# Performance work log

Hardware: AMD Instinct MI355X
Metric: run time of the kernel (lower is better)

The kernel has to match this reference:

```python
import jax, jax.numpy as jnp
import numpy as np

C = 256      # dim_in == dim_out (residual add requires it)
H = 96
W = 96
Z = 16       # number of (isWithin, dist) pairs
MAXL = 8


def setup_inputs() -> dict:
    key = jax.random.key(0)
    ks = jax.random.split(key, 8)
    x = jax.random.normal(ks[0], (1, C, H, W), jnp.float32)
    # 1x1 convs without bias == channel matmuls with weight [out_ch, in_ch]
    Wq = jax.random.normal(ks[1], (C, C), jnp.float32) / np.sqrt(C).astype(np.float32)
    Wk = jax.random.normal(ks[2], (C, C), jnp.float32) / np.sqrt(C).astype(np.float32)
    Wv = jax.random.normal(ks[3], (C, C), jnp.float32) / np.sqrt(C).astype(np.float32)
    embd = jax.random.normal(ks[4], (2, 2 * MAXL + 1, C), jnp.float32)  # N(0,1) as in torch
    Wproj = jax.random.normal(ks[5], (C, C + 1), jnp.float32) / np.sqrt(C + 1).astype(np.float32)
    dist = jax.random.randint(ks[6], (Z,), 0, 2 * MAXL + 1) - MAXL      # in [-maxl, maxl]
    isWithin = jax.random.randint(ks[7], (Z,), 0, 2)                     # in {0, 1}
    return {"x": x, "Wq": Wq, "Wk": Wk, "Wv": Wv, "embd": embd,
            "Wproj": Wproj, "dist": dist, "isWithin": isWithin}


def reference(x, Wq, Wk, Wv, embd, Wproj, dist, isWithin):
    b, c, hh, ww = x.shape
    n = hh * ww
    maxl = (embd.shape[1] - 1) // 2
    xf = x.reshape(b, c, n)                                  # [b, c, n]
    q = jnp.einsum('oc,bcn->bon', Wq, xf)                    # 1x1 conv == channel matmul
    k = jnp.einsum('oc,bcn->bon', Wk, xf)
    v = jnp.einsum('oc,bcn->bon', Wv, xf)
    # full (unscaled) attention over spatial tokens, softmax along q axis
    att = jax.nn.softmax(jnp.einsum('bck,bcq->bkq', k, q), axis=-1)  # [b, n, n]
    Y = jnp.einsum('bkq,bck->bcq', att, v)                   # [b, c, n]
    out = Y.reshape(b, c, hh, ww) + x                        # residual
    # relative-distance embedding gather: [z, c]
    rel = embd[isWithin, dist + maxl]
    pos = jnp.einsum('zc,bcn->bzn', rel, xf)                 # [b, z, n] (u=1 folded)
    pos = pos.reshape(b * pos.shape[1], 1, hh, ww)           # [(b z), 1, hh, ww]
    z = pos.shape[0]
    out_rep = jnp.tile(out, (z, 1, 1, 1))                    # [z, c, hh, ww] (b == 1)
    cat = jnp.concatenate([out_rep, pos], axis=1)            # [z, c+1, hh, ww]
    return jnp.einsum('oc,zchw->zohw', Wproj, cat)           # final 1x1 conv
```

## Files before the change

### kernel.cpp

```cpp
#include <hip/hip_runtime.h>
#include <hip/hip_bf16.h>

typedef __bf16 bf8 __attribute__((ext_vector_type(8)));
typedef __bf16 bfx4 __attribute__((ext_vector_type(4)));
typedef float f4 __attribute__((ext_vector_type(4)));

#define NTOK 9216
#define CDIM 256
#define LOG2E 1.44269504f
#define PSHIFT 32.0f

__device__ inline bf8 ldfrag(const __bf16* p, int ld) {
  int l = threadIdx.x & 63;
  return *reinterpret_cast<const bf8*>(p + (l & 15) * ld + ((l >> 4) << 3));
}
__device__ inline f4 mfma16(bf8 a, bf8 b, f4 c) {
  return __builtin_amdgcn_mfma_f32_16x16x32_bf16(a, b, c, 0, 0, 0);
}
__device__ inline void gl2lds(const __bf16* g, __bf16* l) {
  __builtin_amdgcn_global_load_lds(
      (const __attribute__((address_space(1))) void*)g,
      (__attribute__((address_space(3))) void*)l, 16, 0, 0);
}

template <int EPI>
__global__ __launch_bounds__(256) void gemm128(const __bf16* __restrict__ A, int lda,
                                               const __bf16* __restrict__ Bt, int ldb,
                                               void* __restrict__ Cv, int ldc, int K,
                                               const float* __restrict__ aux0,
                                               const float* __restrict__ aux1) {
  __shared__ __bf16 As[128 * 32];
  __shared__ __bf16 Bs[128 * 32];
  const int tid = threadIdx.x;
  const int w = tid >> 6, lane = tid & 63;
  const int lc = lane & 15, quad = lane >> 4;
  const int m0 = blockIdx.x * 128, n0 = blockIdx.y * 128;
  const int wm = (w & 1) << 6, wn = (w >> 1) << 6;
  const int r0 = (w * 2) * 16 + (lane >> 2);
  const int cg = (lane & 3) * 8;
  const __bf16* gA0 = A + (size_t)(m0 + r0) * lda + cg;
  const __bf16* gA1 = A + (size_t)(m0 + r0 + 16) * lda + cg;
  const __bf16* gB0 = Bt + (size_t)(n0 + r0) * ldb + cg;
  const __bf16* gB1 = Bt + (size_t)(n0 + r0 + 16) * ldb + cg;
  __bf16* lA0 = As + (w * 2) * 512;
  __bf16* lA1 = As + (w * 2 + 1) * 512;
  __bf16* lB0 = Bs + (w * 2) * 512;
  __bf16* lB1 = Bs + (w * 2 + 1) * 512;

  f4 acc[4][4] = {};
  for (int kk = 0; kk < K; kk += 32) {
    __syncthreads();
    gl2lds(gA0 + kk, lA0);
    gl2lds(gA1 + kk, lA1);
    gl2lds(gB0 + kk, lB0);
    gl2lds(gB1 + kk, lB1);
    __syncthreads();
    bf8 af[4], bfr[4];
    for (int i = 0; i < 4; i++) af[i] = ldfrag(As + (wm + 16 * i) * 32, 32);
    for (int j = 0; j < 4; j++) bfr[j] = ldfrag(Bs + (wn + 16 * j) * 32, 32);
    for (int i = 0; i < 4; i++)
      for (int j = 0; j < 4; j++) acc[i][j] = mfma16(af[i], bfr[j], acc[i][j]);
  }
  if (EPI == 3) {
    __bf16* Pp = (__bf16*)Cv;
    float* Pd = (float*)aux0;
    const int mb = blockIdx.x * 2 + (w & 1);
    for (int j = 0; j < 4; j++) {
      int col = n0 + wn + 16 * j + lc;
      int sb = col >> 5, c2 = (col >> 3) & 3, e3 = col & 7;
      float d = 0.f;
      for (int i = 0; i < 4; i++) {
        int qb = m0 + wm + 16 * i + quad * 4;
        for (int r = 0; r < 4; r++) {
          float e = exp2f(acc[i][j][r] - PSHIFT);
          d += e;
          Pp[((size_t)sb * NTOK + qb + r) * 32 + ((c2 ^ r) << 3) + e3] = (__bf16)e;
        }
      }
      d += __shfl_xor(d, 16);
      d += __shfl_xor(d, 32);
      if (quad == 0) Pd[(size_t)col * 144 + mb] = d;
    }
  } else if (EPI == 4) {
    float* outp = (float*)Cv;
    for (int i = 0; i < 4; i++)
      for (int r = 0; r < 4; r++) {
        int o = m0 + wm + 16 * i + quad * 4 + r;
        float wo = aux1[o];
        for (int j = 0; j < 4; j++) {
          int n = n0 + wn + 16 * j + lc;
          float b = acc[i][j][r];
          for (int z = 0; z < 16; z++)
            outp[((size_t)z * 256 + o) * NTOK + n] =
                b + wo * aux0[(size_t)z * NTOK + n];
        }
      }
  } else {
    for (int i = 0; i < 4; i++)
      for (int j = 0; j < 4; j++)
        for (int r = 0; r < 4; r++) {
          size_t idx = (size_t)(m0 + wm + 16 * i + quad * 4 + r) * ldc +
                       (n0 + wn + 16 * j + lc);
          ((__bf16*)Cv)[idx] = (__bf16)acc[i][j][r];
        }
  }
}

__global__ __launch_bounds__(256) void prep_kernel(
    const float* Wq, const float* Wk, const float* Wv, const float* embd,
    const float* Wproj, const int* dist, const int* isWithin,
    __bf16* Wqkb, __bf16* Wvb, __bf16* Wpb, float* wl, __bf16* rel) {
  int tid = blockIdx.x * 256 + threadIdx.x;
  if (tid < 65536) {
    Wqkb[tid] = (__bf16)(Wq[tid] * LOG2E);
    Wqkb[65536 + tid] = (__bf16)Wk[tid];
    Wvb[tid] = (__bf16)Wv[tid];
    int o = tid >> 8, c = tid & 255;
    Wpb[tid] = (__bf16)Wproj[o * 257 + c];
    if (c == 0) wl[o] = Wproj[o * 257 + 256];
  }
  if (tid < 16 * 256) {
    int z = tid >> 8, c = tid & 255;
    rel[tid] = (__bf16)embd[(isWithin[z] * 17 + dist[z] + 8) * 256 + c];
  }
}

__global__ __launch_bounds__(256) void transpose_kernel(const float* x, __bf16* Xt) {
  __shared__ __bf16 tile[32][33];
  int n0 = blockIdx.x * 32;
  int c0 = blockIdx.y * 32;
  int tx = threadIdx.x & 31, ty = threadIdx.x >> 5;
  for (int i = 0; i < 32; i += 8)
    tile[ty + i][tx] = (__bf16)x[(c0 + ty + i) * NTOK + n0 + tx];
  __syncthreads();
  for (int i = 0; i < 32; i += 8)
    Xt[(n0 + ty + i) * CDIM + c0 + tx] = tile[tx][ty + i];
}

__global__ __launch_bounds__(256) void gemm_pos(const __bf16* rel, const __bf16* Xt,
                                                float* pos) {
  int n0 = blockIdx.x * 256 + (threadIdx.x >> 6) * 64;
  f4 acc[4] = {};
  for (int ks = 0; ks < 256; ks += 32) {
    bf8 a = ldfrag(rel + ks, 256);
    for (int j = 0; j < 4; j++) {
      bf8 b = ldfrag(Xt + (n0 + 16 * j) * 256 + ks, 256);
      acc[j] = mfma16(a, b, acc[j]);
    }
  }
  int l = threadIdx.x & 63, lc = l & 15, quad = l >> 4;
  for (int j = 0; j < 4; j++)
    for (int r = 0; r < 4; r++)
      pos[(quad * 4 + r) * NTOK + n0 + 16 * j + lc] = acc[j][r];
}

__global__ __launch_bounds__(256) void combine_stats(const float* __restrict__ Pd,
                                                     float* dinv) {
  int kt = blockIdx.x * 4 + (threadIdx.x >> 6);
  int lane = threadIdx.x & 63;
  const float* pd = Pd + (size_t)kt * 144;
  float d = pd[lane] + pd[lane + 64] + ((lane < 16) ? pd[lane + 128] : 0.f);
  for (int off = 1; off < 64; off <<= 1) d += __shfl_xor(d, off);
  if (lane == 0) dinv[kt] = 1.0f / d;
}

__global__ __launch_bounds__(256) void vscale_kernel(const __bf16* __restrict__ V,
                                                     const float* __restrict__ dinv,
                                                     __bf16* __restrict__ Vs) {
  size_t off = ((size_t)blockIdx.x * 256 + threadIdx.x) * 8;
  bf8 v = *reinterpret_cast<const bf8*>(V + off);
  int c = (int)(off / NTOK);
  int kt = (int)(off % NTOK);
  f4 dl = *reinterpret_cast<const f4*>(dinv + kt);
  f4 dh = *reinterpret_cast<const f4*>(dinv + kt + 4);
  bf8 o;
  for (int j = 0; j < 4; j++) o[j] = (__bf16)((float)v[j] * dl[j]);
  for (int j = 0; j < 4; j++) o[4 + j] = (__bf16)((float)v[4 + j] * dh[j]);
  int c2 = (kt >> 3) & 3;
  size_t dst = (size_t)c * NTOK + (kt & ~31) + (((c2 ^ (c & 3))) << 3);
  *reinterpret_cast<bf8*>(Vs + dst) = o;
}

template <int NSTEP>
__global__ __launch_bounds__(256) void pv_kernel(const __bf16* __restrict__ P,
                                                 const __bf16* __restrict__ Vp,
                                                 float* __restrict__ Ypart) {
  __shared__ __bf16 As[3][64 * 32];
  __shared__ __bf16 Bs[3][256 * 32];
  const int tid = threadIdx.x;
  const int w = tid >> 6, lane = tid & 63;
  const int lc = lane & 15, quad = lane >> 4;
  const int q0 = blockIdx.x * 64;
  const int z = blockIdx.y;
  const int wn = w << 6;
  const int sb0 = z * NSTEP;
  const __bf16* gA = P + ((size_t)sb0 * NTOK + q0) * 32 + w * 512 + lane * 8;
  const size_t aStride = (size_t)NTOK * 32;
  const __bf16* gB = Vp + (size_t)(w * 64 + (lane >> 2)) * NTOK + sb0 * 32 +
                     ((lane & 3) << 3);

  for (int p = 0; p < 2; p++) {
    gl2lds(gA + (size_t)p * aStride, &As[p][w * 512]);
    for (int u = 0; u < 4; u++)
      gl2lds(gB + (size_t)(16 * u) * NTOK + p * 32, &Bs[p][(w * 64 + 16 * u) * 32]);
  }

  f4 acc[4][4] = {};
  int cur = 0;
  const int swz = (quad ^ (lc & 3)) << 3;
  for (int s = 0; s < NSTEP; s++) {
    asm volatile("s_waitcnt vmcnt(5)" ::: "memory");
    __builtin_amdgcn_sched_barrier(0);
    __builtin_amdgcn_s_barrier();
    __builtin_amdgcn_sched_barrier(0);
    int sp = (s + 2 < NSTEP) ? s + 2 : NSTEP - 1;
    int nb = cur + 2;
    if (nb >= 3) nb -= 3;
    gl2lds(gA + (size_t)sp * aStride, &As[nb][w * 512]);
    for (int u = 0; u < 4; u++)
      gl2lds(gB + (size_t)(16 * u) * NTOK + sp * 32, &Bs[nb][(w * 64 + 16 * u) * 32]);
    __builtin_amdgcn_sched_barrier(0);
    bf8 af[4], bfr[4];
    for (int i = 0; i < 4; i++)
      af[i] = *reinterpret_cast<const bf8*>(&As[cur][(16 * i + lc) * 32 + swz]);
    for (int j = 0; j < 4; j++)
      bfr[j] = *reinterpret_cast<const bf8*>(&Bs[cur][(wn + 16 * j + lc) * 32 + swz]);
    for (int i = 0; i < 4; i++)
      for (int j = 0; j < 4; j++) acc[i][j] = mfma16(af[i], bfr[j], acc[i][j]);
    cur = cur + 1;
    if (cur >= 3) cur = 0;
  }

  float* Yp = Ypart + (size_t)z * NTOK * 256;
  for (int i = 0; i < 4; i++)
    for (int j = 0; j < 4; j++)
      for (int r = 0; r < 4; r++)
        Yp[(size_t)(q0 + 16 * i + quad * 4 + r) * 256 + wn + 16 * j + lc] =
            acc[i][j][r];
}

__global__ __launch_bounds__(256) void combine_y_kernel(const float* __restrict__ Ypart,
                                                        const __bf16* __restrict__ Xt,
                                                        __bf16* outT, int zp) {
  int i = blockIdx.x * 256 + threadIdx.x;
  f4 y = {};
  for (int z = 0; z < zp; z++) {
    f4 p = reinterpret_cast<const f4*>(Ypart + (size_t)z * NTOK * 256)[i];
    for (int t = 0; t < 4; t++) y[t] += p[t];
  }
  bfx4 xv = reinterpret_cast<const bfx4*>(Xt)[i];
  bfx4 o;
  for (int t = 0; t < 4; t++) o[t] = (__bf16)(y[t] + (float)xv[t]);
  reinterpret_cast<bfx4*>(outT)[i] = o;
}

extern "C" void kernel_launch(void* const* d_in, const int* in_sizes, int n_in,
                              void* d_out, int out_size, void* d_ws, size_t ws_size,
                              hipStream_t stream) {
  const float* x = (const float*)d_in[0];
  const float* Wq = (const float*)d_in[1];
  const float* Wk = (const float*)d_in[2];
  const float* Wv = (const float*)d_in[3];
  const float* embd = (const float*)d_in[4];
  const float* Wproj = (const float*)d_in[5];
  const int* dist = (const int*)d_in[6];
  const int* isW = (const int*)d_in[7];
  float* out = (float*)d_out;

  char* w8 = (char*)d_ws;
  __bf16* Xt = (__bf16*)(w8 + 0);
  __bf16* QKt = (__bf16*)(w8 + 4718592);
  __bf16* V = (__bf16*)(w8 + 14155776);
  __bf16* Wqkb = (__bf16*)(w8 + 18874368);
  __bf16* Wvb = (__bf16*)(w8 + 19136512);
  __bf16* Wpb = (__bf16*)(w8 + 19267584);
  __bf16* rel = (__bf16*)(w8 + 19398656);
  float* wl = (float*)(w8 + 19406848);
  float* pos = (float*)(w8 + 19407872);
  float* dinv = (float*)(w8 + 20034560);
  __bf16* Vs = (__bf16*)(w8 + 20971520);
  const size_t sOff = 29508608;
  __bf16* P = (__bf16*)(w8 + sOff);
  float* Pd = (float*)(w8 + sOff + 171966464);
  const size_t ypOff = sOff + 171966464 + 5308416;
  float* Ypart = (float*)(w8 + ypOff);
  __bf16* outT = (__bf16*)(w8 + sOff);

  static const int ZPS[] = {6, 4, 3, 2, 1};
  int zp = 1;
  for (int i = 0; i < 5; i++)
    if (ypOff + (size_t)ZPS[i] * 9437184 <= ws_size) { zp = ZPS[i]; break; }

  prep_kernel<<<256, 256, 0, stream>>>(Wq, Wk, Wv, embd, Wproj, dist, isW,
                                       Wqkb, Wvb, Wpb, wl, rel);
  transpose_kernel<<<dim3(288, 8), 256, 0, stream>>>(x, Xt);
  gemm128<1><<<dim3(72, 4), 256, 0, stream>>>(Xt, 256, Wqkb, 256, QKt, 512, 256,
                                              nullptr, nullptr);
  gemm128<1><<<dim3(2, 72), 256, 0, stream>>>(Wvb, 256, Xt, 256, V, NTOK, 256,
                                              nullptr, nullptr);
  gemm_pos<<<36, 256, 0, stream>>>(rel, Xt, pos);
  gemm128<3><<<dim3(72, 72), 256, 0, stream>>>(QKt, 512, QKt + 256, 512, P, 0, 256,
                                               (const float*)Pd, nullptr);
  combine_stats<<<2304, 256, 0, stream>>>(Pd, dinv);
  vscale_kernel<<<1152, 256, 0, stream>>>(V, dinv, Vs);
  switch (zp) {
    case 6: pv_kernel<48><<<dim3(144, 6), 256, 0, stream>>>(P, Vs, Ypart); break;
    case 4: pv_kernel<72><<<dim3(144, 4), 256, 0, stream>>>(P, Vs, Ypart); break;
    case 3: pv_kernel<96><<<dim3(144, 3), 256, 0, stream>>>(P, Vs, Ypart); break;
    case 2: pv_kernel<144><<<dim3(144, 2), 256, 0, stream>>>(P, Vs, Ypart); break;
    default: pv_kernel<288><<<dim3(144, 1), 256, 0, stream>>>(P, Vs, Ypart); break;
  }
  combine_y_kernel<<<2304, 256, 0, stream>>>(Ypart, Xt, outT, zp);
  gemm128<4><<<dim3(2, 72), 256, 0, stream>>>(Wpb, 256, outT, 256, out, NTOK, 256,
                                              pos, wl);
}
```

Before: 408.2 us.

## Stage softmax P tile through LDS for coalesced stores; split final projection across z

The QK^T epilogue now writes exp values into shared memory with an XOR swizzle, in two halves, then each thread stores 16-byte vectors of the P tile to global memory. This replaces scattered 2-byte stores. The final projection GEMM also gets a third grid dimension of 4, so each block writes only 4 of the 16 z outputs, which gives more parallelism for the large output write. The cost is extra barriers and LDS reuse in the epilogue, and the projection GEMM is recomputed 4 times.

```diff
diff --git a/kernel.cpp b/kernel.cpp
--- a/kernel.cpp
+++ b/kernel.cpp
@@ -29,8 +29,9 @@
                                                void* __restrict__ Cv, int ldc, int K,
                                                const float* __restrict__ aux0,
                                                const float* __restrict__ aux1) {
-  __shared__ __bf16 As[128 * 32];
-  __shared__ __bf16 Bs[128 * 32];
+  __shared__ __attribute__((aligned(16))) __bf16 smem[8192];
+  __bf16* As = smem;
+  __bf16* Bs = smem + 4096;
   const int tid = threadIdx.x;
   const int w = tid >> 6, lane = tid & 63;
   const int lc = lane & 15, quad = lane >> 4;
@@ -65,24 +66,39 @@
     __bf16* Pp = (__bf16*)Cv;
     float* Pd = (float*)aux0;
     const int mb = blockIdx.x * 2 + (w & 1);
-    for (int j = 0; j < 4; j++) {
-      int col = n0 + wn + 16 * j + lc;
-      int sb = col >> 5, c2 = (col >> 3) & 3, e3 = col & 7;
-      float d = 0.f;
-      for (int i = 0; i < 4; i++) {
-        int qb = m0 + wm + 16 * i + quad * 4;
-        for (int r = 0; r < 4; r++) {
-          float e = exp2f(acc[i][j][r] - PSHIFT);
-          d += e;
-          Pp[((size_t)sb * NTOK + qb + r) * 32 + ((c2 ^ r) << 3) + e3] = (__bf16)e;
+    for (int p = 0; p < 2; p++) {
+      __syncthreads();
+      if ((w & 1) == p) {
+        for (int j = 0; j < 4; j++) {
+          int cl = wn + 16 * j + lc;
+          int sb = cl >> 5, c2 = (cl >> 3) & 3, e3 = cl & 7;
+          float d = 0.f;
+          for (int i = 0; i < 4; i++)
+            for (int r = 0; r < 4; r++) {
+              float e = exp2f(acc[i][j][r] - PSHIFT);
+              d += e;
+              int rl = 16 * i + quad * 4 + r;
+              smem[rl * 128 + ((sb ^ (r & 3)) << 5) + ((c2 ^ (r & 3)) << 3) + e3] =
+                  (__bf16)e;
+            }
+          d += __shfl_xor(d, 16);
+          d += __shfl_xor(d, 32);
+          if (quad == 0) Pd[(size_t)(n0 + cl) * 144 + mb] = d;
         }
       }
-      d += __shfl_xor(d, 16);
-      d += __shfl_xor(d, 32);
-      if (quad == 0) Pd[(size_t)col * 144 + mb] = d;
+      __syncthreads();
+      int rl = tid >> 2, e = tid & 3;
+      for (int sb = 0; sb < 4; sb++) {
+        bf8 v = *reinterpret_cast<const bf8*>(
+            &smem[rl * 128 + ((sb ^ (rl & 3)) << 5) + e * 8]);
+        *reinterpret_cast<bf8*>(
+            Pp + ((size_t)((n0 >> 5) + sb) * NTOK + m0 + p * 64 + rl) * 32 + e * 8) =
+            v;
+      }
     }
   } else if (EPI == 4) {
     float* outp = (float*)Cv;
+    const int z0 = blockIdx.z * 4;
     for (int i = 0; i < 4; i++)
       for (int r = 0; r < 4; r++) {
         int o = m0 + wm + 16 * i + quad * 4 + r;
@@ -90,7 +106,7 @@
         for (int j = 0; j < 4; j++) {
           int n = n0 + wn + 16 * j + lc;
           float b = acc[i][j][r];
-          for (int z = 0; z < 16; z++)
+          for (int z = z0; z < z0 + 4; z++)
             outp[((size_t)z * 256 + o) * NTOK + n] =
                 b + wo * aux0[(size_t)z * NTOK + n];
         }
@@ -311,6 +327,6 @@
     default: pv_kernel<288><<<dim3(144, 1), 256, 0, stream>>>(P, Vs, Ypart); break;
   }
   combine_y_kernel<<<2304, 256, 0, stream>>>(Ypart, Xt, outT, zp);
-  gemm128<4><<<dim3(2, 72), 256, 0, stream>>>(Wpb, 256, outT, 256, out, NTOK, 256,
-                                              pos, wl);
-}
+  gemm128<4><<<dim3(2, 72, 4), 256, 0, stream>>>(Wpb, 256, outT, 256, out, NTOK, 256,
+                                                 pos, wl);
+}
```

Measured after the change: 416.7 us. 2.1% more time.

## Add pipelined score GEMM with transposed operands and split output GEMM over z

Applied to the files above, without the earlier changes.

Replaces the generic score GEMM epilogue with a dedicated kernel that triple-buffers LDS loads through async global-to-LDS copies and keeps up to two stages in flight. Operands are swapped so each lane writes four exponentials as one packed vector store, and denominators are reduced across lanes in registers. The final projection GEMM grid gains a z dimension of four, so each block writes four z slices and the launch has more parallelism. The cost is extra LDS use and a recomputed projection GEMM in each z block.

```diff
diff --git a/kernel.cpp b/kernel.cpp
--- a/kernel.cpp
+++ b/kernel.cpp
@@ -61,28 +61,9 @@
     for (int i = 0; i < 4; i++)
       for (int j = 0; j < 4; j++) acc[i][j] = mfma16(af[i], bfr[j], acc[i][j]);
   }
-  if (EPI == 3) {
-    __bf16* Pp = (__bf16*)Cv;
-    float* Pd = (float*)aux0;
-    const int mb = blockIdx.x * 2 + (w & 1);
-    for (int j = 0; j < 4; j++) {
-      int col = n0 + wn + 16 * j + lc;
-      int sb = col >> 5, c2 = (col >> 3) & 3, e3 = col & 7;
-      float d = 0.f;
-      for (int i = 0; i < 4; i++) {
-        int qb = m0 + wm + 16 * i + quad * 4;
-        for (int r = 0; r < 4; r++) {
-          float e = exp2f(acc[i][j][r] - PSHIFT);
-          d += e;
-          Pp[((size_t)sb * NTOK + qb + r) * 32 + ((c2 ^ r) << 3) + e3] = (__bf16)e;
-        }
-      }
-      d += __shfl_xor(d, 16);
-      d += __shfl_xor(d, 32);
-      if (quad == 0) Pd[(size_t)col * 144 + mb] = d;
-    }
-  } else if (EPI == 4) {
+  if (EPI == 4) {
     float* outp = (float*)Cv;
+    const int z0 = blockIdx.z * 4;
     for (int i = 0; i < 4; i++)
       for (int r = 0; r < 4; r++) {
         int o = m0 + wm + 16 * i + quad * 4 + r;
@@ -90,7 +71,7 @@
         for (int j = 0; j < 4; j++) {
           int n = n0 + wn + 16 * j + lc;
           float b = acc[i][j][r];
-          for (int z = 0; z < 16; z++)
+          for (int z = z0; z < z0 + 4; z++)
             outp[((size_t)z * 256 + o) * NTOK + n] =
                 b + wo * aux0[(size_t)z * NTOK + n];
         }
@@ -103,6 +84,95 @@
                        (n0 + wn + 16 * j + lc);
           ((__bf16*)Cv)[idx] = (__bf16)acc[i][j][r];
         }
+  }
+}
+
+__global__ __launch_bounds__(256) void sgemm_kernel(const __bf16* __restrict__ Kt,
+                                                    const __bf16* __restrict__ Qt,
+                                                    __bf16* __restrict__ Pp,
+                                                    float* __restrict__ Pd) {
+  __shared__ __bf16 As[3][128 * 32];
+  __shared__ __bf16 Bs[3][128 * 32];
+  const int tid = threadIdx.x;
+  const int w = tid >> 6, lane = tid & 63;
+  const int lc = lane & 15, quad = lane >> 4;
+  const int m0 = blockIdx.x * 128;
+  const int n0 = blockIdx.y * 128;
+  const int wm = (w & 1) << 6, wn = (w >> 1) << 6;
+  const int r0 = w * 32 + (lane >> 2);
+  const int cg = (lane & 3) * 8;
+  const __bf16* gA0 = Kt + (size_t)(m0 + r0) * 512 + cg;
+  const __bf16* gA1 = Kt + (size_t)(m0 + r0 + 16) * 512 + cg;
+  const __bf16* gB0 = Qt + (size_t)(n0 + r0) * 512 + cg;
+  const __bf16* gB1 = Qt + (size_t)(n0 + r0 + 16) * 512 + cg;
+  const int la = w * 1024;
+
+  for (int p = 0; p < 2; p++) {
+    gl2lds(gA0 + p * 32, &As[p][la]);
+    gl2lds(gA1 + p * 32, &As[p][la + 512]);
+    gl2lds(gB0 + p * 32, &Bs[p][la]);
+    gl2lds(gB1 + p * 32, &Bs[p][la + 512]);
+  }
+
+  f4 acc[4][4] = {};
+  int cur = 0;
+  for (int s = 0; s < 8; s++) {
+    asm volatile("s_waitcnt vmcnt(4)" ::: "memory");
+    __builtin_amdgcn_sched_barrier(0);
+    __builtin_amdgcn_s_barrier();
+    __builtin_amdgcn_sched_barrier(0);
+    int sp = (s + 2 < 8) ? s + 2 : 7;
+    int nb = cur + 2;
+    if (nb >= 3) nb -= 3;
+    gl2lds(gA0 + sp * 32, &As[nb][la]);
+    gl2lds(gA1 + sp * 32, &As[nb][la + 512]);
+    gl2lds(gB0 + sp * 32, &Bs[nb][la]);
+    gl2lds(gB1 + sp * 32, &Bs[nb][la + 512]);
+    __builtin_amdgcn_sched_barrier(0);
+    bf8 af[4], bfr[4];
+    for (int i = 0; i < 4; i++) af[i] = ldfrag(&As[cur][(wm + 16 * i) * 32], 32);
+    for (int j = 0; j < 4; j++) bfr[j] = ldfrag(&Bs[cur][(wn + 16 * j) * 32], 32);
+    for (int i = 0; i < 4; i++)
+      for (int j = 0; j < 4; j++) acc[i][j] = mfma16(af[i], bfr[j], acc[i][j]);
+    cur = cur + 1;
+    if (cur >= 3) cur = 0;
+  }
+
+  float dsum[4][4];
+  for (int i = 0; i < 4; i++)
+    for (int r = 0; r < 4; r++) dsum[i][r] = 0.f;
+  for (int j = 0; j < 4; j++) {
+    int q = n0 + wn + 16 * j + lc;
+    for (int i = 0; i < 4; i++) {
+      int ktb = m0 + wm + 16 * i;
+      int c2 = ((i & 1) << 1) | (quad >> 1);
+      bfx4 pk;
+      for (int r = 0; r < 4; r++) {
+        float e = exp2f(acc[i][j][r] - PSHIFT);
+        dsum[i][r] += e;
+        pk[r] = (__bf16)e;
+      }
+      __bf16* dst = Pp + ((size_t)(ktb >> 5) * NTOK + q) * 32 +
+                    ((c2 ^ (lc & 3)) << 3) + ((quad & 1) << 2);
+      *reinterpret_cast<bfx4*>(dst) = pk;
+    }
+  }
+  for (int i = 0; i < 4; i++)
+    for (int r = 0; r < 4; r++) {
+      float d = dsum[i][r];
+      d += __shfl_xor(d, 1);
+      d += __shfl_xor(d, 2);
+      d += __shfl_xor(d, 4);
+      d += __shfl_xor(d, 8);
+      dsum[i][r] = d;
+    }
+  if (lc == 0) {
+    int mb = blockIdx.y * 2 + (w >> 1);
+    for (int i = 0; i < 4; i++)
+      for (int r = 0; r < 4; r++) {
+        int kt = m0 + wm + 16 * i + quad * 4 + r;
+        Pd[(size_t)kt * 144 + mb] = dsum[i][r];
+      }
   }
 }
 
@@ -299,8 +369,7 @@
   gemm128<1><<<dim3(2, 72), 256, 0, stream>>>(Wvb, 256, Xt, 256, V, NTOK, 256,
                                               nullptr, nullptr);
   gemm_pos<<<36, 256, 0, stream>>>(rel, Xt, pos);
-  gemm128<3><<<dim3(72, 72), 256, 0, stream>>>(QKt, 512, QKt + 256, 512, P, 0, 256,
-                                               (const float*)Pd, nullptr);
+  sgemm_kernel<<<dim3(72, 72), 256, 0, stream>>>(QKt + 256, QKt, P, Pd);
   combine_stats<<<2304, 256, 0, stream>>>(Pd, dinv);
   vscale_kernel<<<1152, 256, 0, stream>>>(V, dinv, Vs);
   switch (zp) {
@@ -311,6 +380,6 @@
     default: pv_kernel<288><<<dim3(144, 1), 256, 0, stream>>>(P, Vs, Ypart); break;
   }
   combine_y_kernel<<<2304, 256, 0, stream>>>(Ypart, Xt, outT, zp);
-  gemm128<4><<<dim3(2, 72), 256, 0, stream>>>(Wpb, 256, outT, 256, out, NTOK, 256,
-                                              pos, wl);
-}
+  gemm128<4><<<dim3(2, 72, 4), 256, 0, stream>>>(Wpb, 256, outT, 256, out, NTOK, 256,
+                                                 pos, wl);
+}
```

Result: faster. 399.6 us (-2.1%).
